# Performance work log

Measured on AMD Instinct MI355X. Metric: run time of the kernel, lower is better.

Reference implementation:

```python
import jax, jax.numpy as jnp
import numpy as np

N_HIDDEN = 14  # number of interior Linear(50,50)+ReLU layers (16 Linears total)
WIDTH = 50
IN_DIM = 16
OUT_DIM = 4
BATCH = 2_000_000


def setup_inputs() -> dict:
    key = jax.random.key(0)
    ks = jax.random.split(key, 7)
    s_in = 1.0 / np.sqrt(IN_DIM)
    s_h = 1.0 / np.sqrt(WIDTH)
    x = jax.random.normal(ks[0], (BATCH, IN_DIM), dtype=jnp.float32)
    W0 = jax.random.uniform(ks[1], (WIDTH, IN_DIM), jnp.float32, -s_in, s_in)
    b0 = jax.random.uniform(ks[2], (WIDTH,), jnp.float32, -s_in, s_in)
    Wh = jax.random.uniform(ks[3], (N_HIDDEN, WIDTH, WIDTH), jnp.float32, -s_h, s_h)
    bh = jax.random.uniform(ks[4], (N_HIDDEN, WIDTH), jnp.float32, -s_h, s_h)
    Wo = jax.random.uniform(ks[5], (OUT_DIM, WIDTH), jnp.float32, -s_h, s_h)
    bo = jax.random.uniform(ks[6], (OUT_DIM,), jnp.float32, -s_h, s_h)
    return {"x": x, "W0": W0, "b0": b0, "Wh": Wh, "bh": bh, "Wo": Wo, "bo": bo}


def reference(x, W0, b0, Wh, bh, Wo, bo):
    # first layer: Linear(in,50) + ReLU   (torch Linear: y = x @ W.T + b)
    h = jax.nn.relu(x @ W0.T + b0)

    # 14 hidden Linear(50,50)+ReLU layers via scan over stacked weights
    def layer(h, wb):
        W, b = wb
        return jax.nn.relu(h @ W.T + b), None

    h, _ = jax.lax.scan(layer, h, (Wh, bh))

    # output layer: Linear(50,out), no activation
    return h @ Wo.T + bo
```

## Files before the change

kernel.cpp:

```cpp
#include <hip/hip_runtime.h>
#include <stdint.h>

#define BATCH 2000000
#define NHID  14
#define NT    6
#define NWAVE 12
#define ROWS_PER_BLOCK (NWAVE * 16 * NT)
#define NTILES ((BATCH + ROWS_PER_BLOCK - 1) / ROWS_PER_BLOCK)
#define NSLOT 118
#define LDS_BYTES (NSLOT * 64 * 16)

typedef float    v4f  __attribute__((ext_vector_type(4)));
typedef _Float16 v8h  __attribute__((ext_vector_type(8)));
typedef __fp16   v2p  __attribute__((ext_vector_type(2)));
typedef uint32_t v4u  __attribute__((ext_vector_type(4)));

__device__ __forceinline__ int kown(int kappa) {
    int s = ((kappa >> 5) << 3) | (kappa & 7);
    int q = (kappa >> 3) & 3;
    return ((s >> 2) << 4) | (q * 4 + (s & 3));
}

__device__ __forceinline__ uint32_t pk(float a, float b) {
    union { v2p v; uint32_t u; } c;
    c.v = __builtin_amdgcn_cvt_pkrtz(a, b);
    return c.u;
}
__device__ __forceinline__ uint32_t relu_pk(float a, float b) {
    v2p z = { (__fp16)0.0f, (__fp16)0.0f };
    union { v2p v; uint32_t u; } c;
    c.v = __builtin_amdgcn_cvt_pkrtz(a, b);
    c.v = __builtin_elementwise_max(c.v, z);
    return c.u;
}

__device__ __forceinline__ void pack2(const v4f* acc, v8h* Bv) {
    union { v4u u; v8h h; } c0, c1;
    c0.u.x = relu_pk(acc[0][0], acc[0][1]);
    c0.u.y = relu_pk(acc[0][2], acc[0][3]);
    c0.u.z = relu_pk(acc[1][0], acc[1][1]);
    c0.u.w = relu_pk(acc[1][2], acc[1][3]);
    c1.u.x = relu_pk(acc[2][0], acc[2][1]);
    c1.u.y = relu_pk(acc[2][2], acc[2][3]);
    c1.u.z = relu_pk(acc[3][0], acc[3][1]);
    c1.u.w = relu_pk(acc[3][2], acc[3][3]);
    Bv[0] = c0.h;
    Bv[1] = c1.h;
}

extern "C" __global__ __launch_bounds__(768, 3)
void mlp16(const float* __restrict__ x,
           const float* __restrict__ W0, const float* __restrict__ b0,
           const float* __restrict__ Wh, const float* __restrict__ bh,
           const float* __restrict__ Wo, const float* __restrict__ bo,
           float* __restrict__ out)
{
    extern __shared__ char smem_raw[];
    v8h* frag = (v8h*)smem_raw;

    const int tid  = threadIdx.x;
    const int lane = tid & 63;
    const int wv   = tid >> 6;
    const int l15  = lane & 15;
    const int quad = lane >> 4;

    for (int s = wv; s < NSLOT; s += NWAVE) {
        float v[8];
        if (s < 4) {
            int m = s * 16 + l15;
            #pragma unroll
            for (int j = 0; j < 8; ++j) {
                int kap = quad * 8 + j;
                float val = 0.f;
                if (kap < 16)      { if (m < 50) val = W0[m * 16 + kap]; }
                else if (kap == 16){ if (m < 50) val = b0[m]; else if (m == 50) val = 1.f; }
                v[j] = val;
            }
        } else if (s < 116) {
            int h = s - 4, l = h >> 3, t = (h >> 2) & 1, mt = h & 3;
            int m = mt * 16 + l15;
            const float* W = Wh + l * 2500;
            #pragma unroll
            for (int j = 0; j < 8; ++j) {
                int ko = kown(t * 32 + quad * 8 + j);
                float val = 0.f;
                if (ko < 50)       { if (m < 50) val = W[m * 50 + ko]; }
                else if (ko == 50) { if (m < 50) val = bh[l * 50 + m]; else if (m == 50) val = 1.f; }
                v[j] = val;
            }
        } else {
            int t = s - 116, m = l15;
            #pragma unroll
            for (int j = 0; j < 8; ++j) {
                int ko = kown(t * 32 + quad * 8 + j);
                float val = 0.f;
                if (m < 4) { if (ko < 50) val = Wo[m * 50 + ko]; else if (ko == 50) val = bo[m]; }
                v[j] = val;
            }
        }
        v8h fv;
        #pragma unroll
        for (int j = 0; j < 8; ++j) fv[j] = (_Float16)v[j];
        frag[s * 64 + lane] = fv;
    }
    __syncthreads();

    const v4f z4 = (v4f){0.f, 0.f, 0.f, 0.f};

    for (int tile = blockIdx.x; tile < NTILES; tile += gridDim.x) {
        const int rowbase = tile * ROWS_PER_BLOCK + wv * (16 * NT);
        v8h Bv[NT][2];

        {
            v8h A0[4];
            #pragma unroll
            for (int mt = 0; mt < 4; ++mt) A0[mt] = frag[mt * 64 + lane];
            #pragma unroll
            for (int nt = 0; nt < NT; ++nt) {
                int r  = rowbase + nt * 16 + l15;
                int rc = r < BATCH ? r : BATCH - 1;
                union { v4u u; v8h h; } bx;
                bx.u = (v4u){0u, 0u, 0u, 0u};
                if (quad < 2) {
                    const float* xp = x + (size_t)rc * 16 + quad * 8;
                    v4f xa = *(const v4f*)xp;
                    v4f xb = *(const v4f*)(xp + 4);
                    bx.u.x = pk(xa[0], xa[1]);
                    bx.u.y = pk(xa[2], xa[3]);
                    bx.u.z = pk(xb[0], xb[1]);
                    bx.u.w = pk(xb[2], xb[3]);
                } else if (quad == 2) {
                    bx.u.x = 0x3C00u;
                }
                v4f acc[4];
                #pragma unroll
                for (int mt = 0; mt < 4; ++mt)
                    acc[mt] = __builtin_amdgcn_mfma_f32_16x16x32_f16(A0[mt], bx.h, z4, 0, 0, 0);
                pack2(acc, Bv[nt]);
            }
        }

        for (int l = 0; l < NHID; ++l) {
            v8h A[2][4];
            const v8h* ab = frag + (4 + l * 8) * 64 + lane;
            #pragma unroll
            for (int t = 0; t < 2; ++t)
                #pragma unroll
                for (int mt = 0; mt < 4; ++mt) A[t][mt] = ab[(t * 4 + mt) * 64];
            #pragma unroll
            for (int nt = 0; nt < NT; ++nt) {
                v4f acc[4];
                #pragma unroll
                for (int mt = 0; mt < 4; ++mt)
                    acc[mt] = __builtin_amdgcn_mfma_f32_16x16x32_f16(A[0][mt], Bv[nt][0], z4, 0, 0, 0);
                #pragma unroll
                for (int mt = 0; mt < 4; ++mt)
                    acc[mt] = __builtin_amdgcn_mfma_f32_16x16x32_f16(A[1][mt], Bv[nt][1], acc[mt], 0, 0, 0);
                pack2(acc, Bv[nt]);
            }
        }

        {
            v8h Ao[2];
            #pragma unroll
            for (int t = 0; t < 2; ++t) Ao[t] = frag[(116 + t) * 64 + lane];
            #pragma unroll
            for (int nt = 0; nt < NT; ++nt) {
                v4f acc = __builtin_amdgcn_mfma_f32_16x16x32_f16(Ao[0], Bv[nt][0], z4, 0, 0, 0);
                acc     = __builtin_amdgcn_mfma_f32_16x16x32_f16(Ao[1], Bv[nt][1], acc, 0, 0, 0);
                int r = rowbase + nt * 16 + l15;
                if (quad == 0 && r < BATCH)
                    *(v4f*)(out + (size_t)r * 4) = acc;
            }
        }
    }
}

extern "C" void kernel_launch(void* const* d_in, const int* in_sizes, int n_in,
                              void* d_out, int out_size, void* d_ws, size_t ws_size,
                              hipStream_t stream)
{
    (void)in_sizes; (void)n_in; (void)d_ws; (void)ws_size; (void)out_size;
    (void)hipFuncSetAttribute(reinterpret_cast<const void*>(mlp16),
                              hipFuncAttributeMaxDynamicSharedMemorySize, LDS_BYTES);
    mlp16<<<256, 768, LDS_BYTES, stream>>>(
        (const float*)d_in[0], (const float*)d_in[1], (const float*)d_in[2],
        (const float*)d_in[3], (const float*)d_in[4], (const float*)d_in[5],
        (const float*)d_in[6], (float*)d_out);
}
```

Before: 316.6 us.

## Software-pipeline MFMA chains across row tiles and prefetch next-layer weights

Restructures the hidden-layer loop so the MFMA chains of several row tiles interleave, with pack/ReLU conversions placed between independent MFMAs to hide their dependency latency. Next-layer weight fragments are loaded from LDS during the current layer, and the output-layer weights reuse the same registers. Input loads for all tiles are issued before any conversion so global latency overlaps. The cost is higher register pressure under launch_bounds(768,3), which risks spills or lower occupancy.

```diff
diff --git a/kernel.cpp b/kernel.cpp
--- a/kernel.cpp
+++ b/kernel.cpp
@@ -48,6 +48,18 @@
     Bv[1] = c1.h;
 }
 
+__device__ __forceinline__ void g1(const v8h (&A)[2][4], const v8h* B, v4f (&acc)[4]) {
+    const v4f z4 = (v4f){0.f, 0.f, 0.f, 0.f};
+    #pragma unroll
+    for (int mt = 0; mt < 4; ++mt)
+        acc[mt] = __builtin_amdgcn_mfma_f32_16x16x32_f16(A[0][mt], B[0], z4, 0, 0, 0);
+}
+__device__ __forceinline__ void g2(const v8h (&A)[2][4], const v8h* B, v4f (&acc)[4]) {
+    #pragma unroll
+    for (int mt = 0; mt < 4; ++mt)
+        acc[mt] = __builtin_amdgcn_mfma_f32_16x16x32_f16(A[1][mt], B[1], acc[mt], 0, 0, 0);
+}
+
 extern "C" __global__ __launch_bounds__(768, 3)
 void mlp16(const float* __restrict__ x,
            const float* __restrict__ W0, const float* __restrict__ b0,
@@ -110,25 +122,41 @@
     for (int tile = blockIdx.x; tile < NTILES; tile += gridDim.x) {
         const int rowbase = tile * ROWS_PER_BLOCK + wv * (16 * NT);
         v8h Bv[NT][2];
+        v8h A[2][4];
+
+        {
+            const v8h* ab = frag + 4 * 64 + lane;
+            #pragma unroll
+            for (int t = 0; t < 2; ++t)
+                #pragma unroll
+                for (int mt = 0; mt < 4; ++mt) A[t][mt] = ab[(t * 4 + mt) * 64];
+        }
 
         {
             v8h A0[4];
             #pragma unroll
             for (int mt = 0; mt < 4; ++mt) A0[mt] = frag[mt * 64 + lane];
+
+            v4f xa[NT], xb[NT];
             #pragma unroll
             for (int nt = 0; nt < NT; ++nt) {
                 int r  = rowbase + nt * 16 + l15;
                 int rc = r < BATCH ? r : BATCH - 1;
+                if (quad < 2) {
+                    const float* xp = x + (size_t)rc * 16 + quad * 8;
+                    xa[nt] = *(const v4f*)xp;
+                    xb[nt] = *(const v4f*)(xp + 4);
+                }
+            }
+            #pragma unroll
+            for (int nt = 0; nt < NT; ++nt) {
                 union { v4u u; v8h h; } bx;
                 bx.u = (v4u){0u, 0u, 0u, 0u};
                 if (quad < 2) {
-                    const float* xp = x + (size_t)rc * 16 + quad * 8;
-                    v4f xa = *(const v4f*)xp;
-                    v4f xb = *(const v4f*)(xp + 4);
-                    bx.u.x = pk(xa[0], xa[1]);
-                    bx.u.y = pk(xa[2], xa[3]);
-                    bx.u.z = pk(xb[0], xb[1]);
-                    bx.u.w = pk(xb[2], xb[3]);
+                    bx.u.x = pk(xa[nt][0], xa[nt][1]);
+                    bx.u.y = pk(xa[nt][2], xa[nt][3]);
+                    bx.u.z = pk(xb[nt][0], xb[nt][1]);
+                    bx.u.w = pk(xb[nt][2], xb[nt][3]);
                 } else if (quad == 2) {
                     bx.u.x = 0x3C00u;
                 }
@@ -141,37 +169,52 @@
         }
 
         for (int l = 0; l < NHID; ++l) {
-            v8h A[2][4];
-            const v8h* ab = frag + (4 + l * 8) * 64 + lane;
-            #pragma unroll
-            for (int t = 0; t < 2; ++t)
+            v4f a0[4], a1[4], a2[4], a3[4];
+            g1(A, Bv[0], a0);  g1(A, Bv[1], a1);  g1(A, Bv[2], a2);
+            g2(A, Bv[0], a0);  g2(A, Bv[1], a1);  g2(A, Bv[2], a2);
+            pack2(a0, Bv[0]);  g1(A, Bv[3], a3);
+            pack2(a1, Bv[1]);  g1(A, Bv[4], a0);
+            pack2(a2, Bv[2]);  g1(A, Bv[5], a1);
+            g2(A, Bv[3], a3);  g2(A, Bv[4], a0);  g2(A, Bv[5], a1);
+            if (l + 1 < NHID) {
+                const v8h* ab = frag + (4 + (l + 1) * 8) * 64 + lane;
                 #pragma unroll
-                for (int mt = 0; mt < 4; ++mt) A[t][mt] = ab[(t * 4 + mt) * 64];
-            #pragma unroll
-            for (int nt = 0; nt < NT; ++nt) {
-                v4f acc[4];
-                #pragma unroll
-                for (int mt = 0; mt < 4; ++mt)
-                    acc[mt] = __builtin_amdgcn_mfma_f32_16x16x32_f16(A[0][mt], Bv[nt][0], z4, 0, 0, 0);
-                #pragma unroll
-                for (int mt = 0; mt < 4; ++mt)
-                    acc[mt] = __builtin_amdgcn_mfma_f32_16x16x32_f16(A[1][mt], Bv[nt][1], acc[mt], 0, 0, 0);
-                pack2(acc, Bv[nt]);
-            }
+                for (int t = 0; t < 2; ++t)
+                    #pragma unroll
+                    for (int mt = 0; mt < 4; ++mt) A[t][mt] = ab[(t * 4 + mt) * 64];
+            } else {
+                A[0][0] = frag[116 * 64 + lane];
+                A[0][1] = frag[117 * 64 + lane];
+            }
+            pack2(a3, Bv[3]);  pack2(a0, Bv[4]);  pack2(a1, Bv[5]);
         }
 
         {
-            v8h Ao[2];
-            #pragma unroll
-            for (int t = 0; t < 2; ++t) Ao[t] = frag[(116 + t) * 64 + lane];
-            #pragma unroll
-            for (int nt = 0; nt < NT; ++nt) {
-                v4f acc = __builtin_amdgcn_mfma_f32_16x16x32_f16(Ao[0], Bv[nt][0], z4, 0, 0, 0);
-                acc     = __builtin_amdgcn_mfma_f32_16x16x32_f16(Ao[1], Bv[nt][1], acc, 0, 0, 0);
-                int r = rowbase + nt * 16 + l15;
-                if (quad == 0 && r < BATCH)
-                    *(v4f*)(out + (size_t)r * 4) = acc;
-            }
+            v4f o0, o1, o2;
+            o0 = __builtin_amdgcn_mfma_f32_16x16x32_f16(A[0][0], Bv[0][0], z4, 0, 0, 0);
+            o1 = __builtin_amdgcn_mfma_f32_16x16x32_f16(A[0][0], Bv[1][0], z4, 0, 0, 0);
+            o2 = __builtin_amdgcn_mfma_f32_16x16x32_f16(A[0][0], Bv[2][0], z4, 0, 0, 0);
+            o0 = __builtin_amdgcn_mfma_f32_16x16x32_f16(A[0][1], Bv[0][1], o0, 0, 0, 0);
+            o1 = __builtin_amdgcn_mfma_f32_16x16x32_f16(A[0][1], Bv[1][1], o1, 0, 0, 0);
+            o2 = __builtin_amdgcn_mfma_f32_16x16x32_f16(A[0][1], Bv[2][1], o2, 0, 0, 0);
+            int r0 = rowbase + 0 * 16 + l15;
+            int r1 = rowbase + 1 * 16 + l15;
+            int r2 = rowbase + 2 * 16 + l15;
+            if (quad == 0 && r0 < BATCH) *(v4f*)(out + (size_t)r0 * 4) = o0;
+            if (quad == 0 && r1 < BATCH) *(v4f*)(out + (size_t)r1 * 4) = o1;
+            if (quad == 0 && r2 < BATCH) *(v4f*)(out + (size_t)r2 * 4) = o2;
+            o0 = __builtin_amdgcn_mfma_f32_16x16x32_f16(A[0][0], Bv[3][0], z4, 0, 0, 0);
+            o1 = __builtin_amdgcn_mfma_f32_16x16x32_f16(A[0][0], Bv[4][0], z4, 0, 0, 0);
+            o2 = __builtin_amdgcn_mfma_f32_16x16x32_f16(A[0][0], Bv[5][0], z4, 0, 0, 0);
+            o0 = __builtin_amdgcn_mfma_f32_16x16x32_f16(A[0][1], Bv[3][1], o0, 0, 0, 0);
+            o1 = __builtin_amdgcn_mfma_f32_16x16x32_f16(A[0][1], Bv[4][1], o1, 0, 0, 0);
+            o2 = __builtin_amdgcn_mfma_f32_16x16x32_f16(A[0][1], Bv[5][1], o2, 0, 0, 0);
+            r0 = rowbase + 3 * 16 + l15;
+            r1 = rowbase + 4 * 16 + l15;
+            r2 = rowbase + 5 * 16 + l15;
+            if (quad == 0 && r0 < BATCH) *(v4f*)(out + (size_t)r0 * 4) = o0;
+            if (quad == 0 && r1 < BATCH) *(v4f*)(out + (size_t)r1 * 4) = o1;
+            if (quad == 0 && r2 < BATCH) *(v4f*)(out + (size_t)r2 * 4) = o2;
         }
     }
 }
```

New measurement: 373.3 us. 17.9% more time.

## Switch MFMA tiles from 16x16x32 to 32x32x16 with matching fragment layout

Applied to the files above, without the earlier changes.

Replaces the 16x16x32 f16 MFMA tiling with 32x32x16 instructions. Each wave now handles three 32-row tiles instead of six 16-row tiles, and the LDS weight fragment layout is rewritten to match the new operand layout (120 slots, no kown permutation). The larger MFMA shape is meant to cut instruction count and issue overhead per FLOP. The trade-off is more padding waste, since K=64 and M=64 cover a width of 50, plus longer dependent chains of four accumulations per tile.

```diff
diff --git a/kernel.cpp b/kernel.cpp
--- a/kernel.cpp
+++ b/kernel.cpp
@@ -3,23 +3,19 @@
 
 #define BATCH 2000000
 #define NHID  14
-#define NT    6
 #define NWAVE 12
-#define ROWS_PER_BLOCK (NWAVE * 16 * NT)
+#define ROWS_PER_WAVE 96
+#define ROWS_PER_BLOCK (NWAVE * ROWS_PER_WAVE)
 #define NTILES ((BATCH + ROWS_PER_BLOCK - 1) / ROWS_PER_BLOCK)
-#define NSLOT 118
+#define NSLOT 120
 #define LDS_BYTES (NSLOT * 64 * 16)
 
 typedef float    v4f  __attribute__((ext_vector_type(4)));
+typedef float    v16f __attribute__((ext_vector_type(16)));
 typedef _Float16 v8h  __attribute__((ext_vector_type(8)));
 typedef __fp16   v2p  __attribute__((ext_vector_type(2)));
 typedef uint32_t v4u  __attribute__((ext_vector_type(4)));
 
-__device__ __forceinline__ int kown(int kappa) {
-    int s = ((kappa >> 5) << 3) | (kappa & 7);
-    int q = (kappa >> 3) & 3;
-    return ((s >> 2) << 4) | (q * 4 + (s & 3));
-}
 
 __device__ __forceinline__ uint32_t pk(float a, float b) {
     union { v2p v; uint32_t u; } c;
@@ -34,18 +30,73 @@
     return c.u;
 }
 
-__device__ __forceinline__ void pack2(const v4f* acc, v8h* Bv) {
-    union { v4u u; v8h h; } c0, c1;
-    c0.u.x = relu_pk(acc[0][0], acc[0][1]);
-    c0.u.y = relu_pk(acc[0][2], acc[0][3]);
-    c0.u.z = relu_pk(acc[1][0], acc[1][1]);
-    c0.u.w = relu_pk(acc[1][2], acc[1][3]);
-    c1.u.x = relu_pk(acc[2][0], acc[2][1]);
-    c1.u.y = relu_pk(acc[2][2], acc[2][3]);
-    c1.u.z = relu_pk(acc[3][0], acc[3][1]);
-    c1.u.w = relu_pk(acc[3][2], acc[3][3]);
-    Bv[0] = c0.h;
-    Bv[1] = c1.h;
+__device__ __forceinline__ v16f mfma32(v8h a, v8h b, v16f c) {
+    return __builtin_amdgcn_mfma_f32_32x32x16_f16(a, b, c, 0, 0, 0);
+}
+
+__device__ __forceinline__ v8h pack_lo(const v16f& c) {
+    union { v4u u; v8h h; } r;
+    r.u.x = relu_pk(c[0], c[1]);
+    r.u.y = relu_pk(c[2], c[3]);
+    r.u.z = relu_pk(c[4], c[5]);
+    r.u.w = relu_pk(c[6], c[7]);
+    return r.h;
+}
+__device__ __forceinline__ v8h pack_hi(const v16f& c) {
+    union { v4u u; v8h h; } r;
+    r.u.x = relu_pk(c[8],  c[9]);
+    r.u.y = relu_pk(c[10], c[11]);
+    r.u.z = relu_pk(c[12], c[13]);
+    r.u.w = relu_pk(c[14], c[15]);
+    return r.h;
+}
+
+__device__ __forceinline__ void hidden_tile(const v8h (&A)[8], v8h (&B)[4]) {
+    const v16f z = {0.f,0.f,0.f,0.f,0.f,0.f,0.f,0.f,0.f,0.f,0.f,0.f,0.f,0.f,0.f,0.f};
+    v16f c0 = mfma32(A[0], B[0], z);
+    v16f c1 = mfma32(A[4], B[0], z);
+    c0 = mfma32(A[1], B[1], c0);  c1 = mfma32(A[5], B[1], c1);
+    c0 = mfma32(A[2], B[2], c0);  c1 = mfma32(A[6], B[2], c1);
+    c0 = mfma32(A[3], B[3], c0);  c1 = mfma32(A[7], B[3], c1);
+    B[0] = pack_lo(c0);  B[1] = pack_hi(c0);
+    B[2] = pack_lo(c1);  B[3] = pack_hi(c1);
+}
+
+__device__ __forceinline__ void l0_tile(const v8h (&A0)[4],
+                                        const float* __restrict__ x,
+                                        int r, int hi, v8h (&B)[4]) {
+    int rc = r < BATCH ? r : BATCH - 1;
+    const float* xp = x + (size_t)rc * 16 + hi * 4;
+    v4f xa = *(const v4f*)xp;
+    v4f xb = *(const v4f*)(xp + 8);
+    union { v4u u; v8h h; } b0;
+    b0.u.x = pk(xa[0], xa[1]);
+    b0.u.y = pk(xa[2], xa[3]);
+    b0.u.z = pk(xb[0], xb[1]);
+    b0.u.w = pk(xb[2], xb[3]);
+    union { v4u u; v8h h; } b1;
+    b1.u = (v4u){0u, 0u, 0u, 0u};
+    if (hi == 0) b1.u.x = 0x3C00u;
+    const v16f z = {0.f,0.f,0.f,0.f,0.f,0.f,0.f,0.f,0.f,0.f,0.f,0.f,0.f,0.f,0.f,0.f};
+    v16f c0 = mfma32(A0[0], b0.h, z);
+    v16f c1 = mfma32(A0[2], b0.h, z);
+    c0 = mfma32(A0[1], b1.h, c0);
+    c1 = mfma32(A0[3], b1.h, c1);
+    B[0] = pack_lo(c0);  B[1] = pack_hi(c0);
+    B[2] = pack_lo(c1);  B[3] = pack_hi(c1);
+}
+
+__device__ __forceinline__ void out_tile(const v8h (&Ao)[4], const v8h (&B)[4],
+                                         float* __restrict__ out, int r, int hi) {
+    const v16f z = {0.f,0.f,0.f,0.f,0.f,0.f,0.f,0.f,0.f,0.f,0.f,0.f,0.f,0.f,0.f,0.f};
+    v16f o = mfma32(Ao[0], B[0], z);
+    o = mfma32(Ao[1], B[1], o);
+    o = mfma32(Ao[2], B[2], o);
+    o = mfma32(Ao[3], B[3], o);
+    if (hi == 0 && r < BATCH) {
+        v4f v = {o[0], o[1], o[2], o[3]};
+        *(v4f*)(out + (size_t)r * 4) = v;
+    }
 }
 
 extern "C" __global__ __launch_bounds__(768, 3)
@@ -61,40 +112,41 @@
     const int tid  = threadIdx.x;
     const int lane = tid & 63;
     const int wv   = tid >> 6;
-    const int l15  = lane & 15;
-    const int quad = lane >> 4;
+    const int l31  = lane & 31;
+    const int hi   = lane >> 5;
 
     for (int s = wv; s < NSLOT; s += NWAVE) {
         float v[8];
         if (s < 4) {
-            int m = s * 16 + l15;
+            int sub = s >> 1, t = s & 1;
+            int m = sub * 32 + l31;
             #pragma unroll
             for (int j = 0; j < 8; ++j) {
-                int kap = quad * 8 + j;
+                int f = 16 * t + (j & 3) + 8 * (j >> 2) + 4 * hi;
                 float val = 0.f;
-                if (kap < 16)      { if (m < 50) val = W0[m * 16 + kap]; }
-                else if (kap == 16){ if (m < 50) val = b0[m]; else if (m == 50) val = 1.f; }
+                if (f < 16)       { if (m < 50) val = W0[m * 16 + f]; }
+                else if (f == 16) { if (m < 50) val = b0[m]; else if (m == 50) val = 1.f; }
                 v[j] = val;
             }
         } else if (s < 116) {
-            int h = s - 4, l = h >> 3, t = (h >> 2) & 1, mt = h & 3;
-            int m = mt * 16 + l15;
+            int h = s - 4, l = h >> 3, i = h & 7, sub = i >> 2, t = i & 3;
+            int m = sub * 32 + l31;
             const float* W = Wh + l * 2500;
             #pragma unroll
             for (int j = 0; j < 8; ++j) {
-                int ko = kown(t * 32 + quad * 8 + j);
+                int f = 16 * t + (j & 3) + 8 * (j >> 2) + 4 * hi;
                 float val = 0.f;
-                if (ko < 50)       { if (m < 50) val = W[m * 50 + ko]; }
-                else if (ko == 50) { if (m < 50) val = bh[l * 50 + m]; else if (m == 50) val = 1.f; }
+                if (f < 50)       { if (m < 50) val = W[m * 50 + f]; }
+                else if (f == 50) { if (m < 50) val = bh[l * 50 + m]; else if (m == 50) val = 1.f; }
                 v[j] = val;
             }
         } else {
-            int t = s - 116, m = l15;
+            int t = s - 116, m = l31;
             #pragma unroll
             for (int j = 0; j < 8; ++j) {
-                int ko = kown(t * 32 + quad * 8 + j);
+                int f = 16 * t + (j & 3) + 8 * (j >> 2) + 4 * hi;
                 float val = 0.f;
-                if (m < 4) { if (ko < 50) val = Wo[m * 50 + ko]; else if (ko == 50) val = bo[m]; }
+                if (m < 4) { if (f < 50) val = Wo[m * 50 + f]; else if (f == 50) val = bo[m]; }
                 v[j] = val;
             }
         }
@@ -105,73 +157,36 @@
     }
     __syncthreads();
 
-    const v4f z4 = (v4f){0.f, 0.f, 0.f, 0.f};
-
     for (int tile = blockIdx.x; tile < NTILES; tile += gridDim.x) {
-        const int rowbase = tile * ROWS_PER_BLOCK + wv * (16 * NT);
-        v8h Bv[NT][2];
+        const int rowbase = tile * ROWS_PER_BLOCK + wv * ROWS_PER_WAVE;
+        v8h B0[4], B1[4], B2[4];
 
         {
             v8h A0[4];
             #pragma unroll
-            for (int mt = 0; mt < 4; ++mt) A0[mt] = frag[mt * 64 + lane];
-            #pragma unroll
-            for (int nt = 0; nt < NT; ++nt) {
-                int r  = rowbase + nt * 16 + l15;
-                int rc = r < BATCH ? r : BATCH - 1;
-                union { v4u u; v8h h; } bx;
-                bx.u = (v4u){0u, 0u, 0u, 0u};
-                if (quad < 2) {
-                    const float* xp = x + (size_t)rc * 16 + quad * 8;
-                    v4f xa = *(const v4f*)xp;
-                    v4f xb = *(const v4f*)(xp + 4);
-                    bx.u.x = pk(xa[0], xa[1]);
-                    bx.u.y = pk(xa[2], xa[3]);
-                    bx.u.z = pk(xb[0], xb[1]);
-                    bx.u.w = pk(xb[2], xb[3]);
-                } else if (quad == 2) {
-                    bx.u.x = 0x3C00u;
-                }
-                v4f acc[4];
-                #pragma unroll
-                for (int mt = 0; mt < 4; ++mt)
-                    acc[mt] = __builtin_amdgcn_mfma_f32_16x16x32_f16(A0[mt], bx.h, z4, 0, 0, 0);
-                pack2(acc, Bv[nt]);
-            }
+            for (int i = 0; i < 4; ++i) A0[i] = frag[i * 64 + lane];
+            l0_tile(A0, x, rowbase +  0 + l31, hi, B0);
+            l0_tile(A0, x, rowbase + 32 + l31, hi, B1);
+            l0_tile(A0, x, rowbase + 64 + l31, hi, B2);
         }
 
         for (int l = 0; l < NHID; ++l) {
-            v8h A[2][4];
+            v8h A[8];
             const v8h* ab = frag + (4 + l * 8) * 64 + lane;
             #pragma unroll
-            for (int t = 0; t < 2; ++t)
-                #pragma unroll
-                for (int mt = 0; mt < 4; ++mt) A[t][mt] = ab[(t * 4 + mt) * 64];
-            #pragma unroll
-            for (int nt = 0; nt < NT; ++nt) {
-                v4f acc[4];
-                #pragma unroll
-                for (int mt = 0; mt < 4; ++mt)
-                    acc[mt] = __builtin_amdgcn_mfma_f32_16x16x32_f16(A[0][mt], Bv[nt][0], z4, 0, 0, 0);
-                #pragma unroll
-                for (int mt = 0; mt < 4; ++mt)
-                    acc[mt] = __builtin_amdgcn_mfma_f32_16x16x32_f16(A[1][mt], Bv[nt][1], acc[mt], 0, 0, 0);
-                pack2(acc, Bv[nt]);
-            }
+            for (int i = 0; i < 8; ++i) A[i] = ab[i * 64];
+            hidden_tile(A, B0);
+            hidden_tile(A, B1);
+            hidden_tile(A, B2);
         }
 
         {
-            v8h Ao[2];
-            #pragma unroll
-            for (int t = 0; t < 2; ++t) Ao[t] = frag[(116 + t) * 64 + lane];
-            #pragma unroll
-            for (int nt = 0; nt < NT; ++nt) {
-                v4f acc = __builtin_amdgcn_mfma_f32_16x16x32_f16(Ao[0], Bv[nt][0], z4, 0, 0, 0);
-                acc     = __builtin_amdgcn_mfma_f32_16x16x32_f16(Ao[1], Bv[nt][1], acc, 0, 0, 0);
-                int r = rowbase + nt * 16 + l15;
-                if (quad == 0 && r < BATCH)
-                    *(v4f*)(out + (size_t)r * 4) = acc;
-            }
+            v8h Ao[4];
+            #pragma unroll
+            for (int i = 0; i < 4; ++i) Ao[i] = frag[(116 + i) * 64 + lane];
+            out_tile(Ao, B0, out, rowbase +  0 + l31, hi);
+            out_tile(Ao, B1, out, rowbase + 32 + l31, hi);
+            out_tile(Ao, B2, out, rowbase + 64 + l31, hi);
         }
     }
 }
```

After: 318.7 us. No clear change (+0.7%).
